# Kernel tuning notes

Measured on AMD Instinct MI355X. Metric: run time of the kernel, lower is better.

## Reference

```python
import jax, jax.numpy as jnp
import numpy as np

WS = 8          # window size M
SHIFT = WS // 2 # cyclic shift
HEADS = 8


def _rel_pos_index(ws):
    # (ws*ws, ws*ws) indices into the (2ws-1)^2 bias table
    coords = np.stack(np.meshgrid(np.arange(ws), np.arange(ws), indexing='ij'), 0).reshape(2, -1)
    rel = coords[:, :, None] - coords[:, None, :]          # (2, N, N)
    rel = rel.transpose(1, 2, 0) + (ws - 1)                # shift to [0, 2ws-2]
    return rel[..., 0] * (2 * ws - 1) + rel[..., 1]        # (N, N)


def _shift_mask(H, W, ws, shift):
    # standard Swin attention mask for shifted windows: (nWin, N, N)
    img = np.zeros((H, W), dtype=np.int32)
    cnt = 0
    for hs in (slice(0, -ws), slice(-ws, -shift), slice(-shift, None)):
        for wsl in (slice(0, -ws), slice(-ws, -shift), slice(-shift, None)):
            img[hs, wsl] = cnt
            cnt += 1
    mw = img.reshape(H // ws, ws, W // ws, ws).transpose(0, 2, 1, 3).reshape(-1, ws * ws)
    diff = mw[:, None, :] - mw[:, :, None]
    return np.where(diff != 0, -100.0, 0.0).astype(np.float32)


def setup_inputs() -> dict:
    key = jax.random.key(0)
    ks = jax.random.split(key, 6)
    B, C, H, W = 32, 256, 64, 64
    return {
        'x': jax.random.normal(ks[0], (B, C, H, W), jnp.float32),
        'w_qkv': jax.random.normal(ks[1], (C, 3 * C), jnp.float32) * (C ** -0.5),
        'b_qkv': jnp.zeros((3 * C,), jnp.float32),
        'w_o': jax.random.normal(ks[2], (C, C), jnp.float32) * (C ** -0.5),
        'b_o': jnp.zeros((C,), jnp.float32),
        'rel_bias_table': jax.random.normal(ks[3], ((2 * WS - 1) ** 2, HEADS), jnp.float32) * 0.02,
    }


def reference(x, w_qkv, b_qkv, w_o, b_o, rel_bias_table):
    B, C, H, W = x.shape
    ws, shift, heads = WS, SHIFT, HEADS
    dh = C // heads
    nH, nW = H // ws, W // ws
    nWin, N = nH * nW, ws * ws

    rel_idx = jnp.asarray(_rel_pos_index(ws))                 # (N, N) int
    mask = jnp.asarray(_shift_mask(H, W, ws, shift))          # (nWin, N, N)

    # cyclic shift
    xs = jnp.roll(x, (-shift, -shift), axis=(2, 3))
    # window partition: (B, C, H, W) -> (B, nWin, N, C)
    xw = xs.reshape(B, C, nH, ws, nW, ws).transpose(0, 2, 4, 3, 5, 1).reshape(B, nWin, N, C)

    qkv = xw @ w_qkv + b_qkv                                  # (B, nWin, N, 3C)
    qkv = qkv.reshape(B, nWin, N, 3, heads, dh)
    q = qkv[..., 0, :, :].transpose(0, 1, 3, 2, 4)            # (B, nWin, h, N, dh)
    k = qkv[..., 1, :, :].transpose(0, 1, 3, 2, 4)
    v = qkv[..., 2, :, :].transpose(0, 1, 3, 2, 4)

    attn = jnp.einsum('bwhnd,bwhmd->bwhnm', q, k) * (dh ** -0.5)
    bias = rel_bias_table[rel_idx]                            # (N, N, heads)
    attn = attn + bias.transpose(2, 0, 1)[None, None]         # add rel pos bias
    attn = attn + mask[None, :, None]                         # add shift mask
    attn = jax.nn.softmax(attn, axis=-1)

    out = jnp.einsum('bwhnm,bwhmd->bwhnd', attn, v)           # (B, nWin, h, N, dh)
    out = out.transpose(0, 1, 3, 2, 4).reshape(B, nWin, N, C)
    out = out @ w_o + b_o

    # window reverse: (B, nWin, N, C) -> (B, C, H, W)
    out = out.reshape(B, nH, nW, ws, ws, C).transpose(0, 5, 1, 3, 2, 4).reshape(B, C, H, W)
    # reverse cyclic shift
    return jnp.roll(out, (shift, shift), axis=(2, 3))
```

## Files before the change

kernel.cpp:

```cpp
#include <hip/hip_runtime.h>
#include <stdint.h>

typedef __attribute__((ext_vector_type(8))) short short8;
typedef __attribute__((ext_vector_type(4))) float floatx4;
typedef unsigned short u16;
typedef unsigned int u32;

#define MFMA16(a,b,c) __builtin_amdgcn_mfma_f32_16x16x32_bf16((a),(b),(c),0,0,0)

__device__ __forceinline__ u16 f2b(float f){
  u32 i; __builtin_memcpy(&i,&f,4); i += 0x7FFFu + ((i>>16)&1u); return (u16)(i>>16);
}
__device__ __forceinline__ int regid(int p){ return (p<56)?0:((p<60)?1:2); }

#define SCO 16896
#define LDS_ELEMS 26112

__global__ void prep_w(const float* __restrict__ wqkv, const float* __restrict__ wo,
                       u16* __restrict__ wqkvT, u16* __restrict__ woT){
  int idx = blockIdx.x*256 + threadIdx.x;
  if(idx < 768*256){ int n = idx>>8, k = idx&255; wqkvT[idx] = f2b(wqkv[k*768 + n]); }
  else { int j = idx - 768*256; int n = j>>8, k = j&255; woT[j] = f2b(wo[k*256 + n]); }
}

__global__ __launch_bounds__(256,3) void swmsa_fused(
    const float* __restrict__ x, const u16* __restrict__ wqkvT, const float* __restrict__ bqkv,
    const u16* __restrict__ woT, const float* __restrict__ bo, const float* __restrict__ table,
    float* __restrict__ out)
{
  extern __shared__ u16 lds[];
  const int tid  = threadIdx.x;
  const int wave = tid>>6, lane = tid&63;
  const int quad = lane>>4, colid = lane&15;
  const int bi = blockIdx.x;
  const int xcd = bi & 7, j = bi >> 3;
  const int r0 = ((j >> 3) << 3) | xcd;
  const int wx = j & 7;
  const int b = r0 >> 3, wy = r0 & 7;
  const size_t imgbase = (size_t)b*256*4096;
  const int w0 = wx*8+4;
  const floatx4 fzero = {0.f,0.f,0.f,0.f};
  u16* sc = lds + SCO + wave*2304;

  for(int i=0;i<2;++i){
    int unit = tid + 256*i;
    int cg = unit>>3, ty = unit&7;
    int hs = (wy*8+ty+4)&63;
    u16 vv[4][8];
    #pragma unroll
    for(int cc=0;cc<4;++cc){
      const float* src = x + imgbase + (size_t)(cg*4+cc)*4096 + (size_t)hs*64;
      floatx4 lo, hi;
      if(wx<7){ lo = *(const floatx4*)(src+w0); hi = *(const floatx4*)(src+w0+4); }
      else    { lo = *(const floatx4*)(src+60); hi = *(const floatx4*)(src); }
      #pragma unroll
      for(int t=0;t<4;++t){ vv[cc][t]=f2b(lo[t]); vv[cc][4+t]=f2b(hi[t]); }
    }
    #pragma unroll
    for(int t=0;t<8;++t){
      uint64_t pk = (uint64_t)vv[0][t] | ((uint64_t)vv[1][t]<<16)
                  | ((uint64_t)vv[2][t]<<32) | ((uint64_t)vv[3][t]<<48);
      *(uint64_t*)&lds[(ty*8+t)*264 + cg*4] = pk;
    }
  }
  __syncthreads();

  short8 aq2[2][4], bk2[2][4], bv2[2][2][2];
  for(int t3=0; t3<3; ++t3){
    const int cc = 2 - t3;
    const int col0 = (cc*4 + wave)*64;
    const u16* wslab = wqkvT + (size_t)(col0+colid)*256 + quad*8;
    floatx4 acc[4][4];
    #pragma unroll
    for(int mt=0;mt<4;++mt)
      #pragma unroll
      for(int nt=0;nt<4;++nt) acc[mt][nt] = fzero;
    short8 bcur[4], bnxt[4];
    #pragma unroll
    for(int nt=0;nt<4;++nt) bcur[nt] = *(const short8*)&wslab[(size_t)nt*16*256];
    for(int k0=0;k0<256;k0+=32){
      short8 af[4];
      #pragma unroll
      for(int mt=0;mt<4;++mt) af[mt]  = *(const short8*)&lds[(mt*16+colid)*264 + k0 + quad*8];
      if(k0 < 224){
        #pragma unroll
        for(int nt=0;nt<4;++nt) bnxt[nt] = *(const short8*)&wslab[(size_t)nt*16*256 + k0 + 32];
      }
      #pragma unroll
      for(int mt=0;mt<4;++mt)
        #pragma unroll
        for(int nt=0;nt<4;++nt) acc[mt][nt] = MFMA16(af[mt], bcur[nt], acc[mt][nt]);
      #pragma unroll
      for(int nt=0;nt<4;++nt) bcur[nt] = bnxt[nt];
    }
    #pragma unroll
    for(int hf=0; hf<2; ++hf){
      #pragma unroll
      for(int nt2=0; nt2<2; ++nt2){
        int nt = hf*2 + nt2;
        float bias = bqkv[col0 + nt*16 + colid];
        #pragma unroll
        for(int mt=0;mt<4;++mt)
          #pragma unroll
          for(int rr=0;rr<4;++rr){
            int row = mt*16 + quad*4 + rr;
            u16 bvv = f2b(acc[mt][nt][rr] + bias);
            if(cc==2) sc[(nt2*16+colid)*72 + row] = bvv;
            else      sc[row*36 + nt2*16 + colid] = bvv;
          }
      }
      if(cc==2){
        #pragma unroll
        for(int n2=0;n2<2;++n2)
          #pragma unroll
          for(int kc=0;kc<2;++kc)
            bv2[hf][n2][kc] = *(const short8*)&sc[(n2*16+colid)*72 + kc*32 + quad*8];
      } else if(cc==1){
        #pragma unroll
        for(int mt=0;mt<4;++mt) bk2[hf][mt] = *(const short8*)&sc[(mt*16+colid)*36 + quad*8];
      } else {
        #pragma unroll
        for(int mt=0;mt<4;++mt) aq2[hf][mt] = *(const short8*)&sc[(mt*16+colid)*36 + quad*8];
      }
    }
  }
  __syncthreads();

  const float scale = 0.17677669529663687f;
  #pragma unroll
  for(int hi=0; hi<2; ++hi){
    const int h = wave*2 + hi;
    floatx4 s[4][4];
    #pragma unroll
    for(int mt=0;mt<4;++mt)
      #pragma unroll
      for(int nt=0;nt<4;++nt) s[mt][nt] = MFMA16(aq2[hi][mt], bk2[hi][nt], fzero);
    int cntk[4], kys[4], kxs[4];
    #pragma unroll
    for(int nt=0;nt<4;++nt){
      int col = nt*16 + colid;
      kys[nt] = col>>3; kxs[nt] = col&7;
      cntk[nt] = regid(wy*8 + kys[nt])*3 + regid(wx*8 + kxs[nt]);
    }
    #pragma unroll
    for(int mt=0;mt<4;++mt)
      #pragma unroll
      for(int rr=0;rr<4;++rr){
        int row = mt*16 + quad*4 + rr;
        int ty = row>>3, tx = row&7;
        int cntq = regid(wy*8+ty)*3 + regid(wx*8+tx);
        #pragma unroll
        for(int nt=0;nt<4;++nt){
          int rel = (ty - kys[nt] + 7)*15 + (tx - kxs[nt] + 7);
          float add = table[rel*8 + h] + ((cntq==cntk[nt]) ? 0.f : -100.f);
          s[mt][nt][rr] = s[mt][nt][rr]*scale + add;
        }
      }
    u32 gpk[4][4];
    #pragma unroll
    for(int mt=0;mt<4;++mt)
      #pragma unroll
      for(int rr=0;rr<4;++rr){
        float mx = s[mt][0][rr];
        #pragma unroll
        for(int nt=1;nt<4;++nt) mx = fmaxf(mx, s[mt][nt][rr]);
        #pragma unroll
        for(int d=1; d<16; d<<=1) mx = fmaxf(mx, __shfl_xor(mx, d));
        float e[4], sum = 0.f;
        #pragma unroll
        for(int nt=0;nt<4;++nt){ e[nt] = __expf(s[mt][nt][rr]-mx); sum += e[nt]; }
        #pragma unroll
        for(int d=1; d<16; d<<=1) sum += __shfl_xor(sum, d);
        float inv = 1.0f/sum;
        int row = mt*16 + quad*4 + rr;
        sc[row*36 + colid]      = f2b(e[0]*inv);
        sc[row*36 + 16 + colid] = f2b(e[1]*inv);
        gpk[mt][rr] = (u32)f2b(e[2]*inv) | ((u32)f2b(e[3]*inv) << 16);
      }
    floatx4 o[4][2];
    #pragma unroll
    for(int mt=0;mt<4;++mt){ o[mt][0]=fzero; o[mt][1]=fzero; }
    #pragma unroll
    for(int kc=0;kc<2;++kc){
      if(kc==1){
        #pragma unroll
        for(int mt=0;mt<4;++mt)
          #pragma unroll
          for(int rr=0;rr<4;++rr){
            int row = mt*16 + quad*4 + rr;
            sc[row*36 + colid]      = (u16)(gpk[mt][rr] & 0xffffu);
            sc[row*36 + 16 + colid] = (u16)(gpk[mt][rr] >> 16);
          }
      }
      short8 ap[4];
      #pragma unroll
      for(int mt=0;mt<4;++mt) ap[mt] = *(const short8*)&sc[(mt*16+colid)*36 + quad*8];
      #pragma unroll
      for(int mt=0;mt<4;++mt)
        #pragma unroll
        for(int n2=0;n2<2;++n2) o[mt][n2] = MFMA16(ap[mt], bv2[hi][n2][kc], o[mt][n2]);
    }
    #pragma unroll
    for(int n2=0;n2<2;++n2){
      int c = h*32 + n2*16 + colid;
      #pragma unroll
      for(int mt=0;mt<4;++mt)
        #pragma unroll
        for(int rr=0;rr<4;++rr)
          lds[(mt*16+quad*4+rr)*264 + c] = f2b(o[mt][n2][rr]);
    }
  }
  __syncthreads();

  {
    floatx4 acc[4][4];
    #pragma unroll
    for(int np=0;np<4;++np)
      #pragma unroll
      for(int mt=0;mt<4;++mt) acc[np][mt] = fzero;
    const u16* wbase = woT + (size_t)(wave*16+colid)*256 + quad*8;
    for(int k0=0;k0<256;k0+=32){
      short8 ay[4];
      #pragma unroll
      for(int mt=0;mt<4;++mt) ay[mt] = *(const short8*)&lds[(mt*16+colid)*264 + k0 + quad*8];
      #pragma unroll
      for(int np=0;np<4;++np){
        short8 bw = *(const short8*)&wbase[(size_t)np*16384 + k0];
        #pragma unroll
        for(int mt=0;mt<4;++mt) acc[np][mt] = MFMA16(ay[mt], bw, acc[np][mt]);
      }
    }
    const int ty_base = quad>>1, txg = quad&1;
    const int col = (wx<7) ? (w0 + 4*txg) : (txg ? 0 : 60);
    #pragma unroll
    for(int np=0;np<4;++np){
      const int ch = np*64 + wave*16 + colid;
      const float bias = bo[ch];
      float* chbase = out + imgbase + (size_t)ch*4096;
      #pragma unroll
      for(int mt=0;mt<4;++mt){
        int ty = 2*mt + ty_base;
        int hd = (wy*8 + ty + 4) & 63;
        floatx4 vsto = acc[np][mt];
        vsto[0]+=bias; vsto[1]+=bias; vsto[2]+=bias; vsto[3]+=bias;
        *(floatx4*)(chbase + (size_t)hd*64 + col) = vsto;
      }
    }
  }
}

extern "C" void kernel_launch(void* const* d_in, const int* in_sizes, int n_in,
                              void* d_out, int out_size, void* d_ws, size_t ws_size,
                              hipStream_t stream) {
  const float* x     = (const float*)d_in[0];
  const float* wqkv  = (const float*)d_in[1];
  const float* bqkv  = (const float*)d_in[2];
  const float* wo    = (const float*)d_in[3];
  const float* bo    = (const float*)d_in[4];
  const float* table = (const float*)d_in[5];
  float* out = (float*)d_out;

  u16* wqkvT = (u16*)d_ws;
  u16* woT   = wqkvT + 768*256;

  prep_w<<<1024, 256, 0, stream>>>(wqkv, wo, wqkvT, woT);

  (void)hipFuncSetAttribute((const void*)swmsa_fused,
                            hipFuncAttributeMaxDynamicSharedMemorySize, LDS_ELEMS*2);
  swmsa_fused<<<2048, 256, LDS_ELEMS*2, stream>>>(x, wqkvT, bqkv, woT, bo, table, out);
}
```

Baseline: 479.3 us.

## Split fused Swin attention into attention kernel and separate output-projection GEMM

Splits the single fused kernel into two. The first computes window attention and writes a bf16 intermediate to workspace, laid out in band order. The second does the output projection with a double-buffered, swizzled LDS tile over 256-token bands, which gives better weight reuse and coalesced row stores. The aim is to drop the projection's register and LDS pressure from the attention kernel, at the cost of an extra global round trip (about 67MB of bf16) and one more launch. It falls back to the fused path if the workspace is too small.

```diff
diff --git a/kernel.cpp b/kernel.cpp
--- a/kernel.cpp
+++ b/kernel.cpp
@@ -21,6 +21,274 @@
   int idx = blockIdx.x*256 + threadIdx.x;
   if(idx < 768*256){ int n = idx>>8, k = idx&255; wqkvT[idx] = f2b(wqkv[k*768 + n]); }
   else { int j = idx - 768*256; int n = j>>8, k = j&255; woT[j] = f2b(wo[k*256 + n]); }
+}
+
+__global__ __launch_bounds__(256,3) void swmsa_attn(
+    const float* __restrict__ x, const u16* __restrict__ wqkvT, const float* __restrict__ bqkv,
+    const float* __restrict__ table, u16* __restrict__ yws)
+{
+  extern __shared__ u16 lds[];
+  const int tid  = threadIdx.x;
+  const int wave = tid>>6, lane = tid&63;
+  const int quad = lane>>4, colid = lane&15;
+  const int bi = blockIdx.x;
+  const int xcd = bi & 7, j = bi >> 3;
+  const int r0 = ((j >> 3) << 3) | xcd;
+  const int wx = j & 7;
+  const int b = r0 >> 3, wy = r0 & 7;
+  const size_t imgbase = (size_t)b*256*4096;
+  const int w0 = wx*8+4;
+  const floatx4 fzero = {0.f,0.f,0.f,0.f};
+  u16* sc = lds + SCO + wave*2304;
+
+  for(int i=0;i<2;++i){
+    int unit = tid + 256*i;
+    int cg = unit>>3, ty = unit&7;
+    int hs = (wy*8+ty+4)&63;
+    u16 vv[4][8];
+    #pragma unroll
+    for(int cc=0;cc<4;++cc){
+      const float* src = x + imgbase + (size_t)(cg*4+cc)*4096 + (size_t)hs*64;
+      floatx4 lo, hi;
+      if(wx<7){ lo = *(const floatx4*)(src+w0); hi = *(const floatx4*)(src+w0+4); }
+      else    { lo = *(const floatx4*)(src+60); hi = *(const floatx4*)(src); }
+      #pragma unroll
+      for(int t=0;t<4;++t){ vv[cc][t]=f2b(lo[t]); vv[cc][4+t]=f2b(hi[t]); }
+    }
+    #pragma unroll
+    for(int t=0;t<8;++t){
+      uint64_t pk = (uint64_t)vv[0][t] | ((uint64_t)vv[1][t]<<16)
+                  | ((uint64_t)vv[2][t]<<32) | ((uint64_t)vv[3][t]<<48);
+      *(uint64_t*)&lds[(ty*8+t)*264 + cg*4] = pk;
+    }
+  }
+  __syncthreads();
+
+  short8 aq2[2][4], bk2[2][4], bv2[2][2][2];
+  for(int t3=0; t3<3; ++t3){
+    const int cc = 2 - t3;
+    const int col0 = (cc*4 + wave)*64;
+    const u16* wslab = wqkvT + (size_t)(col0+colid)*256 + quad*8;
+    floatx4 acc[4][4];
+    #pragma unroll
+    for(int mt=0;mt<4;++mt)
+      #pragma unroll
+      for(int nt=0;nt<4;++nt) acc[mt][nt] = fzero;
+    short8 bcur[4], bnxt[4];
+    #pragma unroll
+    for(int nt=0;nt<4;++nt) bcur[nt] = *(const short8*)&wslab[(size_t)nt*16*256];
+    for(int k0=0;k0<256;k0+=32){
+      short8 af[4];
+      #pragma unroll
+      for(int mt=0;mt<4;++mt) af[mt]  = *(const short8*)&lds[(mt*16+colid)*264 + k0 + quad*8];
+      if(k0 < 224){
+        #pragma unroll
+        for(int nt=0;nt<4;++nt) bnxt[nt] = *(const short8*)&wslab[(size_t)nt*16*256 + k0 + 32];
+      }
+      #pragma unroll
+      for(int mt=0;mt<4;++mt)
+        #pragma unroll
+        for(int nt=0;nt<4;++nt) acc[mt][nt] = MFMA16(af[mt], bcur[nt], acc[mt][nt]);
+      #pragma unroll
+      for(int nt=0;nt<4;++nt) bcur[nt] = bnxt[nt];
+    }
+    #pragma unroll
+    for(int hf=0; hf<2; ++hf){
+      #pragma unroll
+      for(int nt2=0; nt2<2; ++nt2){
+        int nt = hf*2 + nt2;
+        float bias = bqkv[col0 + nt*16 + colid];
+        #pragma unroll
+        for(int mt=0;mt<4;++mt)
+          #pragma unroll
+          for(int rr=0;rr<4;++rr){
+            int row = mt*16 + quad*4 + rr;
+            u16 bvv = f2b(acc[mt][nt][rr] + bias);
+            if(cc==2) sc[(nt2*16+colid)*72 + row] = bvv;
+            else      sc[row*36 + nt2*16 + colid] = bvv;
+          }
+      }
+      if(cc==2){
+        #pragma unroll
+        for(int n2=0;n2<2;++n2)
+          #pragma unroll
+          for(int kc=0;kc<2;++kc)
+            bv2[hf][n2][kc] = *(const short8*)&sc[(n2*16+colid)*72 + kc*32 + quad*8];
+      } else if(cc==1){
+        #pragma unroll
+        for(int mt=0;mt<4;++mt) bk2[hf][mt] = *(const short8*)&sc[(mt*16+colid)*36 + quad*8];
+      } else {
+        #pragma unroll
+        for(int mt=0;mt<4;++mt) aq2[hf][mt] = *(const short8*)&sc[(mt*16+colid)*36 + quad*8];
+      }
+    }
+  }
+  __syncthreads();
+
+  const float scale = 0.17677669529663687f;
+  #pragma unroll
+  for(int hi=0; hi<2; ++hi){
+    const int h = wave*2 + hi;
+    floatx4 s[4][4];
+    #pragma unroll
+    for(int mt=0;mt<4;++mt)
+      #pragma unroll
+      for(int nt=0;nt<4;++nt) s[mt][nt] = MFMA16(aq2[hi][mt], bk2[hi][nt], fzero);
+    int cntk[4], kys[4], kxs[4];
+    #pragma unroll
+    for(int nt=0;nt<4;++nt){
+      int col = nt*16 + colid;
+      kys[nt] = col>>3; kxs[nt] = col&7;
+      cntk[nt] = regid(wy*8 + kys[nt])*3 + regid(wx*8 + kxs[nt]);
+    }
+    #pragma unroll
+    for(int mt=0;mt<4;++mt)
+      #pragma unroll
+      for(int rr=0;rr<4;++rr){
+        int row = mt*16 + quad*4 + rr;
+        int ty = row>>3, tx = row&7;
+        int cntq = regid(wy*8+ty)*3 + regid(wx*8+tx);
+        #pragma unroll
+        for(int nt=0;nt<4;++nt){
+          int rel = (ty - kys[nt] + 7)*15 + (tx - kxs[nt] + 7);
+          float add = table[rel*8 + h] + ((cntq==cntk[nt]) ? 0.f : -100.f);
+          s[mt][nt][rr] = s[mt][nt][rr]*scale + add;
+        }
+      }
+    u32 gpk[4][4];
+    #pragma unroll
+    for(int mt=0;mt<4;++mt)
+      #pragma unroll
+      for(int rr=0;rr<4;++rr){
+        float mx = s[mt][0][rr];
+        #pragma unroll
+        for(int nt=1;nt<4;++nt) mx = fmaxf(mx, s[mt][nt][rr]);
+        #pragma unroll
+        for(int d=1; d<16; d<<=1) mx = fmaxf(mx, __shfl_xor(mx, d));
+        float e[4], sum = 0.f;
+        #pragma unroll
+        for(int nt=0;nt<4;++nt){ e[nt] = __expf(s[mt][nt][rr]-mx); sum += e[nt]; }
+        #pragma unroll
+        for(int d=1; d<16; d<<=1) sum += __shfl_xor(sum, d);
+        float inv = 1.0f/sum;
+        int row = mt*16 + quad*4 + rr;
+        sc[row*36 + colid]      = f2b(e[0]*inv);
+        sc[row*36 + 16 + colid] = f2b(e[1]*inv);
+        gpk[mt][rr] = (u32)f2b(e[2]*inv) | ((u32)f2b(e[3]*inv) << 16);
+      }
+    floatx4 o[4][2];
+    #pragma unroll
+    for(int mt=0;mt<4;++mt){ o[mt][0]=fzero; o[mt][1]=fzero; }
+    #pragma unroll
+    for(int kc=0;kc<2;++kc){
+      if(kc==1){
+        #pragma unroll
+        for(int mt=0;mt<4;++mt)
+          #pragma unroll
+          for(int rr=0;rr<4;++rr){
+            int row = mt*16 + quad*4 + rr;
+            sc[row*36 + colid]      = (u16)(gpk[mt][rr] & 0xffffu);
+            sc[row*36 + 16 + colid] = (u16)(gpk[mt][rr] >> 16);
+          }
+      }
+      short8 ap[4];
+      #pragma unroll
+      for(int mt=0;mt<4;++mt) ap[mt] = *(const short8*)&sc[(mt*16+colid)*36 + quad*8];
+      #pragma unroll
+      for(int mt=0;mt<4;++mt)
+        #pragma unroll
+        for(int n2=0;n2<2;++n2) o[mt][n2] = MFMA16(ap[mt], bv2[hi][n2][kc], o[mt][n2]);
+    }
+    #pragma unroll
+    for(int n2=0;n2<2;++n2){
+      int c = h*32 + n2*16 + colid;
+      #pragma unroll
+      for(int mt=0;mt<4;++mt)
+        #pragma unroll
+        for(int rr=0;rr<4;++rr)
+          lds[(mt*16+quad*4+rr)*264 + c] = f2b(o[mt][n2][rr]);
+    }
+  }
+  __syncthreads();
+
+  const size_t bandbase = (size_t)r0 * (512*256);
+  #pragma unroll
+  for(int i=0;i<8;++i){
+    int unit = i*256 + tid;
+    int tokw = unit>>5, c8 = unit&31;
+    int tyw = tokw>>3, txw = tokw&7;
+    int cg = (8*wx + 4 + txw) & 63;
+    size_t t = (size_t)(tyw*64 + cg);
+    *(short8*)&yws[bandbase + t*256 + c8*8] = *(const short8*)&lds[tokw*264 + c8*8];
+  }
+}
+
+__global__ __launch_bounds__(256,3) void swmsa_proj(
+    const u16* __restrict__ yws, const u16* __restrict__ woT,
+    const float* __restrict__ bo, float* __restrict__ out)
+{
+  __shared__ u16 tile[2][256*32];
+  const int tid = threadIdx.x;
+  const int wave = tid>>6, lane = tid&63;
+  const int quad = lane>>4, colid = lane&15;
+  const int bi = blockIdx.x;
+  const int x7 = bi&7, jj = bi>>3;
+  const int band = ((jj>>3)<<3) | x7;
+  const int sub = jj&7, h2 = sub>>2, npp = sub&3;
+  const int b = band>>3, wy = band&7;
+  const u16* ybase = yws + (size_t)band*(512*256) + (size_t)h2*(256*256);
+  const int ch = npp*64 + wave*16 + colid;
+  const u16* wbase = woT + (size_t)ch*256 + quad*8;
+  const floatx4 fzero = {0.f,0.f,0.f,0.f};
+  floatx4 acc[16];
+  #pragma unroll
+  for(int mt=0;mt<16;++mt) acc[mt]=fzero;
+
+  const int rbase0 = tid>>2, slot = tid&3;
+  const int swz = (tid>>3)&3;
+  const int rsw = (colid>>1)&3;
+
+  short8 sv[4];
+  #pragma unroll
+  for(int i=0;i<4;++i)
+    sv[i] = *(const short8*)&ybase[(size_t)(i*64 + rbase0)*256 + slot*8];
+  #pragma unroll
+  for(int i=0;i<4;++i)
+    *(short8*)&tile[0][(i*64+rbase0)*32 + ((slot^swz))*8] = sv[i];
+  __syncthreads();
+
+  for(int kk=0;kk<8;++kk){
+    const int cur = kk&1;
+    if(kk<7){
+      #pragma unroll
+      for(int i=0;i<4;++i)
+        sv[i] = *(const short8*)&ybase[(size_t)(i*64 + rbase0)*256 + (kk+1)*32 + slot*8];
+    }
+    short8 bw = *(const short8*)&wbase[kk*32];
+    #pragma unroll
+    for(int mt=0;mt<16;++mt){
+      short8 a = *(const short8*)&tile[cur][(mt*16+colid)*32 + ((quad^rsw))*8];
+      acc[mt] = MFMA16(a, bw, acc[mt]);
+    }
+    if(kk<7){
+      #pragma unroll
+      for(int i=0;i<4;++i)
+        *(short8*)&tile[cur^1][(i*64+rbase0)*32 + ((slot^swz))*8] = sv[i];
+    }
+    __syncthreads();
+  }
+
+  const float bias = bo[ch];
+  float* obase = out + (size_t)b*256*4096 + (size_t)ch*4096;
+  #pragma unroll
+  for(int mt=0;mt<16;++mt){
+    int ty = mt>>2;
+    int hd = (wy*8 + h2*4 + ty + 4) & 63;
+    int colb = (mt&3)*16 + quad*4;
+    floatx4 v = acc[mt];
+    v[0]+=bias; v[1]+=bias; v[2]+=bias; v[3]+=bias;
+    *(floatx4*)(obase + (size_t)hd*64 + colb) = v;
+  }
 }
 
 __global__ __launch_bounds__(256,3) void swmsa_fused(
@@ -240,7 +508,7 @@
       #pragma unroll
       for(int mt=0;mt<4;++mt){
         int ty = 2*mt + ty_base;
-        int hd = (wy*8 + ty + 4) & 63;
+        int hd = (wy*8 + ty + 4)&63;
         floatx4 vsto = acc[np][mt];
         vsto[0]+=bias; vsto[1]+=bias; vsto[2]+=bias; vsto[3]+=bias;
         *(floatx4*)(chbase + (size_t)hd*64 + col) = vsto;
@@ -262,10 +530,20 @@
 
   u16* wqkvT = (u16*)d_ws;
   u16* woT   = wqkvT + 768*256;
+  u16* yws   = woT   + 256*256;
+
+  const size_t need = (size_t)(768*256 + 256*256)*2 + (size_t)256*512*256*2;
 
   prep_w<<<1024, 256, 0, stream>>>(wqkv, wo, wqkvT, woT);
 
-  (void)hipFuncSetAttribute((const void*)swmsa_fused,
-                            hipFuncAttributeMaxDynamicSharedMemorySize, LDS_ELEMS*2);
-  swmsa_fused<<<2048, 256, LDS_ELEMS*2, stream>>>(x, wqkvT, bqkv, woT, bo, table, out);
+  if(ws_size >= need){
+    (void)hipFuncSetAttribute((const void*)swmsa_attn,
+                              hipFuncAttributeMaxDynamicSharedMemorySize, LDS_ELEMS*2);
+    swmsa_attn<<<2048, 256, LDS_ELEMS*2, stream>>>(x, wqkvT, bqkv, table, yws);
+    swmsa_proj<<<2048, 256, 0, stream>>>(yws, woT, bo, out);
+  } else {
+    (void)hipFuncSetAttribute((const void*)swmsa_fused,
+                              hipFuncAttributeMaxDynamicSharedMemorySize, LDS_ELEMS*2);
+    swmsa_fused<<<2048, 256, LDS_ELEMS*2, stream>>>(x, wqkvT, bqkv, woT, bo, table, out);
+  }
 }
```

Result: no change. 473.6 us (-1.2%).
